# Kernel tuning notes

Measured on AMD Instinct MI355X. Metric: run time of the kernel, lower is better.

Reference implementation:

```python
import jax, jax.numpy as jnp
import numpy as np

D_MODEL = 768
N_HEADS = 12
D_K = D_MODEL // N_HEADS


def setup_inputs() -> dict:
    key = jax.random.key(0)
    ks = jax.random.split(key, 11)
    B, S, D = 8, 1024, D_MODEL
    std = 1.0 / np.sqrt(D)
    inp = {
        "key": jax.random.normal(ks[0], (B, S, D), jnp.float32),
        "query": jax.random.normal(ks[1], (B, S, D), jnp.float32),
        "value": jax.random.normal(ks[2], (B, S, D), jnp.float32),
        # torch.nn.Linear weights are [out, in]; y = x @ W.T + b
        "Wk": jax.random.uniform(ks[3], (D, D), jnp.float32, -std, std),
        "bk": jax.random.uniform(ks[4], (D,), jnp.float32, -std, std),
        "Wq": jax.random.uniform(ks[5], (D, D), jnp.float32, -std, std),
        "bq": jax.random.uniform(ks[6], (D,), jnp.float32, -std, std),
        "Wv": jax.random.uniform(ks[7], (D, D), jnp.float32, -std, std),
        "bv": jax.random.uniform(ks[8], (D,), jnp.float32, -std, std),
        "Wo": jax.random.uniform(ks[9], (D, D), jnp.float32, -std, std),
        "bo": jax.random.uniform(ks[10], (D,), jnp.float32, -std, std),
    }
    return inp


def _split_heads(x):
    B, S, D = x.shape
    return x.reshape(B, S, N_HEADS, D_K).transpose(0, 2, 1, 3)  # [B,H,S,d_k]


def reference(key, query, value, Wk, bk, Wq, bq, Wv, bv, Wo, bo):
    k = _split_heads(key @ Wk.T + bk)
    q = _split_heads(query @ Wq.T + bq)
    v = _split_heads(value @ Wv.T + bv)
    scores = jnp.einsum("bhqd,bhkd->bhqk", q, k) / jnp.sqrt(jnp.float32(D_K))
    attn = jax.nn.softmax(scores, axis=-1)
    out = jnp.einsum("bhqk,bhkd->bhqd", attn, v)  # [B,H,S,d_k]
    B, H, S, dk = out.shape
    concat = out.transpose(0, 2, 1, 3).reshape(B, S, H * dk)
    return concat @ Wo.T + bo
```

## Files before the change

kernel.cpp:

```cpp
#include <hip/hip_runtime.h>
#include <stdint.h>

#define DI __device__ __forceinline__

typedef __attribute__((ext_vector_type(8))) __bf16 bfrag;
typedef __attribute__((ext_vector_type(4))) __bf16 bf16x4;
typedef __attribute__((ext_vector_type(4))) float f32x4;

static constexpr int Bb = 8, Ss = 1024, Dd = 768, Hh = 12, DKk = 64;
static constexpr int Mm = Bb * Ss;

typedef __attribute__((address_space(3))) void lds_void_t;
typedef const __attribute__((address_space(1))) void gvoid_t;

DI void async_load16(const void* g, void* lds) {
    __builtin_amdgcn_global_load_lds((gvoid_t*)(uintptr_t)g,
                                     (lds_void_t*)(uint32_t)(uintptr_t)lds, 16, 0, 0);
}

#if __has_builtin(__builtin_amdgcn_exp2f)
#define EXP2(x) __builtin_amdgcn_exp2f(x)
#else
extern "C" __device__ float __ocml_exp2_f32(float);
#define EXP2(x) __ocml_exp2_f32(x)
#endif

__global__ __launch_bounds__(256) void cvt_k(const float* __restrict__ a0, const float* __restrict__ a1,
                                             const float* __restrict__ a2,
                                             const float* __restrict__ w0, const float* __restrict__ w1,
                                             const float* __restrict__ w2, const float* __restrict__ w3,
                                             __bf16* __restrict__ da0, __bf16* __restrict__ da1,
                                             __bf16* __restrict__ da2,
                                             __bf16* __restrict__ dw0, __bf16* __restrict__ dw1,
                                             __bf16* __restrict__ dw2, __bf16* __restrict__ dw3) {
    const int bid = (int)blockIdx.x;
    const float* s; __bf16* d; int off;
    if (bid < 9216) {
        const int ti = bid / 3072;
        off = (bid % 3072) * 2048;
        s = ti == 0 ? a0 : ti == 1 ? a1 : a2;
        d = ti == 0 ? da0 : ti == 1 ? da1 : da2;
    } else {
        const int b2 = bid - 9216;
        const int ti = b2 / 288;
        off = (b2 % 288) * 2048;
        s = ti == 0 ? w0 : ti == 1 ? w1 : ti == 2 ? w2 : w3;
        d = ti == 0 ? dw0 : ti == 1 ? dw1 : ti == 2 ? dw2 : dw3;
    }
    const int i = off + (int)threadIdx.x * 8;
    f32x4 a = *(const f32x4*)(s + i);
    f32x4 b = *(const f32x4*)(s + i + 4);
    bfrag o;
#pragma unroll
    for (int j = 0; j < 4; ++j) { o[j] = (__bf16)a[j]; o[j + 4] = (__bf16)b[j]; }
    *(bfrag*)(d + i) = o;
}

DI void gemm_core8(const __bf16* __restrict__ A, const __bf16* __restrict__ W,
                   __bf16* As, __bf16* Bs, int row0, int col0, int t, f32x4 acc[4][2]) {
    const int lane = t & 63, w = t >> 6;
    const int l15 = lane & 15, lg = lane >> 4;
    const int wr = (w >> 2) * 64, wc = (w & 3) * 32;
    const int rl = lane >> 3, clin = lane & 7;

    for (int k0 = 0; k0 < 768; k0 += 64) {
        __syncthreads();
#pragma unroll
        for (int o = 0; o < 2; ++o) {
            const int g = w * 2 + o;
            const int r = g * 8 + rl;
            const int cg = clin ^ (r & 7);
            async_load16(A + (size_t)(row0 + r) * Dd + k0 + cg * 8, As + g * 512);
            async_load16(W + (size_t)(col0 + r) * Dd + k0 + cg * 8, Bs + g * 512);
        }
        __syncthreads();

        bfrag af[4][2], bf[2][2];
#pragma unroll
        for (int mi = 0; mi < 4; ++mi) {
            const int ra = wr + mi * 16 + l15;
#pragma unroll
            for (int ks = 0; ks < 2; ++ks)
                af[mi][ks] = *(const bfrag*)(As + ra * 64 + (((ks * 4 + lg) ^ (ra & 7)) * 8));
        }
#pragma unroll
        for (int ni = 0; ni < 2; ++ni) {
            const int rb = wc + ni * 16 + l15;
#pragma unroll
            for (int ks = 0; ks < 2; ++ks)
                bf[ni][ks] = *(const bfrag*)(Bs + rb * 64 + (((ks * 4 + lg) ^ (rb & 7)) * 8));
        }
#pragma unroll
        for (int mi = 0; mi < 4; ++mi)
#pragma unroll
            for (int ni = 0; ni < 2; ++ni)
#pragma unroll
                for (int ks = 0; ks < 2; ++ks)
                    acc[mi][ni] = __builtin_amdgcn_mfma_f32_16x16x32_bf16(af[mi][ks], bf[ni][ks],
                                                                          acc[mi][ni], 0, 0, 0);
    }
}

__global__ __launch_bounds__(512) void qkv_gemm(const __bf16* __restrict__ qA, const __bf16* __restrict__ kA,
                                                const __bf16* __restrict__ vA,
                                                const __bf16* __restrict__ qW, const __bf16* __restrict__ kW,
                                                const __bf16* __restrict__ vW,
                                                const float* __restrict__ qb, const float* __restrict__ kb,
                                                const float* __restrict__ vb,
                                                __bf16* __restrict__ qO, __bf16* __restrict__ kO,
                                                __bf16* __restrict__ vO) {
    __shared__ __attribute__((aligned(16))) char smem[32768];
    __bf16* As = (__bf16*)smem;
    __bf16* Bs = (__bf16*)(smem + 16384);

    const int h = (int)blockIdx.x;
    const int l = (h & 7) * 144 + (h >> 3);
    const int z = l / 384, r2 = l % 384;
    const int row0 = (r2 / 6) * 128, col0 = (r2 % 6) * 128;

    const __bf16* A = z == 0 ? qA : z == 1 ? kA : vA;
    const __bf16* W = z == 0 ? qW : z == 1 ? kW : vW;
    const float* bias = z == 0 ? qb : z == 1 ? kb : vb;
    __bf16* O = z == 0 ? qO : z == 1 ? kO : vO;

    const int t = (int)threadIdx.x;
    const int lane = t & 63, w = t >> 6;
    const int l15 = lane & 15, lg = lane >> 4;
    const int wr = (w >> 2) * 64, wc = (w & 3) * 32;

    f32x4 acc[4][2] = {};
    gemm_core8(A, W, As, Bs, row0, col0, t, acc);

    if (z == 2) {
        auto T = reinterpret_cast<__bf16(*)[136]>(smem);
        const int bb2 = row0 >> 10, sb = row0 & 1023;
#pragma unroll
        for (int dh = 0; dh < 2; ++dh) {
            __syncthreads();
            if (((w >> 1) & 1) == dh) {
#pragma unroll
                for (int mi = 0; mi < 4; ++mi)
#pragma unroll
                    for (int ni = 0; ni < 2; ++ni) {
                        const int dcol = (w & 1) * 32 + ni * 16 + l15;
                        const float bv = bias[col0 + dh * 64 + dcol];
#pragma unroll
                        for (int j = 0; j < 4; ++j)
                            T[dcol][wr + mi * 16 + lg * 4 + j] = (__bf16)(acc[mi][ni][j] + bv);
                    }
            }
            __syncthreads();
#pragma unroll
            for (int it = 0; it < 2; ++it) {
                const int ld = it * 32 + (t >> 4);
                const int cs = (t & 15) * 8;
                const int col = col0 + dh * 64 + ld;
                const int head = col >> 6, dd = col & 63;
                __bf16* dst = O + ((size_t)(bb2 * Hh + head) * DKk + dd) * Ss + sb + cs;
                *reinterpret_cast<bfrag*>(dst) = *reinterpret_cast<const bfrag*>(&T[ld][cs]);
            }
        }
    } else {
        const float scl = (z == 0) ? 0.18033688f : 1.0f;
#pragma unroll
        for (int mi = 0; mi < 4; ++mi) {
#pragma unroll
            for (int ni = 0; ni < 2; ++ni) {
                const int cg = col0 + wc + ni * 16 + l15;
                const float bv = bias[cg];
#pragma unroll
                for (int j = 0; j < 4; ++j) {
                    const int rg = row0 + wr + mi * 16 + lg * 4 + j;
                    const float val = (acc[mi][ni][j] + bv) * scl;
                    const int bb = rg >> 10, ss = rg & 1023;
                    const int hh2 = cg >> 6, dd = cg & 63;
                    O[((size_t)(bb * Hh + hh2) * Ss + ss) * DKk + dd] = (__bf16)val;
                }
            }
        }
    }
}

__global__ __launch_bounds__(512) void o_gemm(const __bf16* __restrict__ A, const __bf16* __restrict__ W,
                                              const float* __restrict__ bias, float* __restrict__ Out) {
    __shared__ __attribute__((aligned(16))) char smem[24576];
    __bf16* As = (__bf16*)smem;
    __bf16* Bs = (__bf16*)(smem + 16384);

    const int h = (int)blockIdx.x;
    const int l = (h & 7) * 96 + (h >> 3);
    const int row0 = (l / 12) * 128, col0 = (l % 12) * 64;

    const int t = (int)threadIdx.x;
    const int lane = t & 63, w = t >> 6;
    const int l15 = lane & 15, lg = lane >> 4;
    const int wr = (w >> 1) * 32, wc = (w & 1) * 32;
    const int rl = lane >> 3, clin = lane & 7;

    f32x4 acc[2][2] = {};

    for (int k0 = 0; k0 < 768; k0 += 64) {
        __syncthreads();
#pragma unroll
        for (int o = 0; o < 2; ++o) {
            const int g = w * 2 + o;
            const int r = g * 8 + rl;
            const int cg = clin ^ (r & 7);
            async_load16(A + (size_t)(row0 + r) * Dd + k0 + cg * 8, As + g * 512);
        }
        {
            const int r = w * 8 + rl;
            const int cg = clin ^ (r & 7);
            async_load16(W + (size_t)(col0 + r) * Dd + k0 + cg * 8, Bs + w * 512);
        }
        __syncthreads();

        bfrag af[2][2], bf[2][2];
#pragma unroll
        for (int mi = 0; mi < 2; ++mi) {
            const int ra = wr + mi * 16 + l15;
#pragma unroll
            for (int ks = 0; ks < 2; ++ks)
                af[mi][ks] = *(const bfrag*)(As + ra * 64 + (((ks * 4 + lg) ^ (ra & 7)) * 8));
        }
#pragma unroll
        for (int ni = 0; ni < 2; ++ni) {
            const int rb = wc + ni * 16 + l15;
#pragma unroll
            for (int ks = 0; ks < 2; ++ks)
                bf[ni][ks] = *(const bfrag*)(Bs + rb * 64 + (((ks * 4 + lg) ^ (rb & 7)) * 8));
        }
#pragma unroll
        for (int mi = 0; mi < 2; ++mi)
#pragma unroll
            for (int ni = 0; ni < 2; ++ni)
#pragma unroll
                for (int ks = 0; ks < 2; ++ks)
                    acc[mi][ni] = __builtin_amdgcn_mfma_f32_16x16x32_bf16(af[mi][ks], bf[ni][ks],
                                                                          acc[mi][ni], 0, 0, 0);
    }

#pragma unroll
    for (int mi = 0; mi < 2; ++mi) {
#pragma unroll
        for (int ni = 0; ni < 2; ++ni) {
            const int cg = col0 + wc + ni * 16 + l15;
            const float bv = bias[cg];
#pragma unroll
            for (int j = 0; j < 4; ++j) {
                const int rg = row0 + wr + mi * 16 + lg * 4 + j;
                Out[(size_t)rg * Dd + cg] = acc[mi][ni][j] + bv;
            }
        }
    }
}

__global__ __launch_bounds__(512) void attn_k(const __bf16* __restrict__ q,
                                              const __bf16* __restrict__ k,
                                              const __bf16* __restrict__ vt,
                                              __bf16* __restrict__ o) {
    __shared__ __attribute__((aligned(16))) __bf16 Ks[64][72];
    __shared__ __attribute__((aligned(16))) __bf16 Vs[64][72];
    __shared__ __attribute__((aligned(16))) __bf16 plds[8][16][72];
    const int t = (int)threadIdx.x;
    const int lane = t & 63, w = t >> 6;
    const int l15 = lane & 15, lg = lane >> 4;
    const int blk = (int)blockIdx.x;
    const int bh = blk % 96, qt = blk / 96;
    const size_t bhb = (size_t)bh * Ss;
    const __bf16* qp = q + bhb * DKk;
    const __bf16* kp = k + bhb * DKk;
    const __bf16* vtp = vt + bhb * DKk;
    const int qbase = qt * 128 + w * 16;
    const int srow = t >> 3, sc = (t & 7) * 8;

    bfrag bq[2];
#pragma unroll
    for (int ks = 0; ks < 2; ++ks)
        bq[ks] = *reinterpret_cast<const bfrag*>(qp + (size_t)(qbase + l15) * DKk + ks * 32 + lg * 8);

    float lpart = 0.f;
    f32x4 oacc[4] = {};

    {
        bfrag k0 = *reinterpret_cast<const bfrag*>(kp + (size_t)srow * DKk + sc);
        bfrag v0 = *reinterpret_cast<const bfrag*>(vtp + (size_t)srow * Ss + sc);
        *reinterpret_cast<bfrag*>(&Ks[srow][sc]) = k0;
        *reinterpret_cast<bfrag*>(&Vs[srow][sc]) = v0;
    }
    __syncthreads();

    for (int kt = 0; kt < 16; ++kt) {
        bfrag kn, vn;
        if (kt < 15) {
            const int kb1 = (kt + 1) * 64;
            kn = *reinterpret_cast<const bfrag*>(kp + (size_t)(kb1 + srow) * DKk + sc);
            vn = *reinterpret_cast<const bfrag*>(vtp + (size_t)srow * Ss + kb1 + sc);
        }

        f32x4 sacc[4] = {};
        __builtin_amdgcn_s_setprio(1);
#pragma unroll
        for (int n = 0; n < 4; ++n) {
#pragma unroll
            for (int ks = 0; ks < 2; ++ks) {
                const bfrag ak = *reinterpret_cast<const bfrag*>(&Ks[n * 16 + l15][ks * 32 + lg * 8]);
                sacc[n] = __builtin_amdgcn_mfma_f32_16x16x32_bf16(ak, bq[ks], sacc[n], 0, 0, 0);
            }
        }
        __builtin_amdgcn_s_setprio(0);

        __syncthreads();
        if (kt < 15)
            *reinterpret_cast<bfrag*>(&Ks[srow][sc]) = kn;

        float p[4][4];
        float rs = 0.f;
#pragma unroll
        for (int n = 0; n < 4; ++n)
#pragma unroll
            for (int j = 0; j < 4; ++j) {
                const float pe = EXP2(sacc[n][j]);
                p[n][j] = pe;
                rs += pe;
            }
        lpart += rs;

#pragma unroll
        for (int n = 0; n < 4; ++n) {
            bf16x4 pk;
#pragma unroll
            for (int j = 0; j < 4; ++j) pk[j] = (__bf16)p[n][j];
            *reinterpret_cast<bf16x4*>(&plds[w][l15][n * 16 + lg * 4]) = pk;
        }

        __builtin_amdgcn_s_setprio(1);
#pragma unroll
        for (int ks = 0; ks < 2; ++ks) {
            const bfrag ap = *reinterpret_cast<const bfrag*>(&plds[w][l15][ks * 32 + lg * 8]);
#pragma unroll
            for (int dt = 0; dt < 4; ++dt) {
                const bfrag bv = *reinterpret_cast<const bfrag*>(&Vs[dt * 16 + l15][ks * 32 + lg * 8]);
                oacc[dt] = __builtin_amdgcn_mfma_f32_16x16x32_bf16(ap, bv, oacc[dt], 0, 0, 0);
            }
        }
        __builtin_amdgcn_s_setprio(0);

        __syncthreads();
        if (kt < 15)
            *reinterpret_cast<bfrag*>(&Vs[srow][sc]) = vn;
    }

    float lrow = lpart;
    lrow += __shfl_xor(lrow, 16);
    lrow += __shfl_xor(lrow, 32);
    float linv[4];
#pragma unroll
    for (int j = 0; j < 4; ++j) linv[j] = 1.0f / __shfl(lrow, lg * 4 + j);
    const int bb = bh / Hh, hh = bh % Hh;
#pragma unroll
    for (int dt = 0; dt < 4; ++dt)
#pragma unroll
        for (int j = 0; j < 4; ++j) {
            const int qrow = qbase + lg * 4 + j;
            o[((size_t)(bb * Ss + qrow)) * Dd + hh * DKk + dt * 16 + l15] =
                (__bf16)(oacc[dt][j] * linv[j]);
        }
}

extern "C" void kernel_launch(void* const* d_in, const int* in_sizes, int n_in,
                              void* d_out, int out_size, void* d_ws, size_t ws_size,
                              hipStream_t stream) {
    (void)in_sizes; (void)n_in; (void)out_size; (void)ws_size;
    const float* key   = (const float*)d_in[0];
    const float* query = (const float*)d_in[1];
    const float* value = (const float*)d_in[2];
    const float* Wk = (const float*)d_in[3];
    const float* bk = (const float*)d_in[4];
    const float* Wq = (const float*)d_in[5];
    const float* bq = (const float*)d_in[6];
    const float* Wv = (const float*)d_in[7];
    const float* bvp = (const float*)d_in[8];
    const float* Wo = (const float*)d_in[9];
    const float* bo = (const float*)d_in[10];

    const size_t NA = (size_t)Mm * Dd;
    const size_t NW = (size_t)Dd * Dd;
    __bf16* p = (__bf16*)d_ws;
    __bf16* qab = p;            p += NA;
    __bf16* kab = p;            p += NA;
    __bf16* vab = p;            p += NA;
    __bf16* wqb = p;            p += NW;
    __bf16* wkb = p;            p += NW;
    __bf16* wvb = p;            p += NW;
    __bf16* wob = p;            p += NW;
    __bf16* qws = p;            p += NA;
    __bf16* kws = p;            p += NA;
    __bf16* vtws = p;           p += NA;
    __bf16* aws = qab;

    dim3 b256(256), b512(512);
    cvt_k<<<dim3(10368), b256, 0, stream>>>(query, key, value, Wq, Wk, Wv, Wo,
                                            qab, kab, vab, wqb, wkb, wvb, wob);
    qkv_gemm<<<dim3(1152), b512, 0, stream>>>(qab, kab, vab,
                                              wqb, wkb, wvb,
                                              bq, bk, bvp,
                                              qws, kws, vtws);
    attn_k<<<dim3(Ss / 128 * Hh * Bb), b512, 0, stream>>>(qws, kws, vtws, aws);
    o_gemm<<<dim3(768), b512, 0, stream>>>(aws, wob, bo, (float*)d_out);
}
```

Baseline: 109.1 us.

## Fuse fp32-to-bf16 activation conversion into QKV GEMM A-tile loads

The separate conversion pass over the three fp32 activation tensors is removed. The QKV GEMM now reads fp32 activations directly, converts them to bf16 in registers and writes them swizzled into LDS, while weights are still pre-converted and loaded asynchronously. This saves a full write and re-read of three bf16 activation copies. The cost is that A-tile loads become synchronous register loads rather than async global-to-LDS copies, and each GEMM block re-reads and re-converts fp32 data across its six column tiles.

After: 110.2 us. No clear change (+1.0%).

```diff
diff --git a/kernel.cpp b/kernel.cpp
--- a/kernel.cpp
+++ b/kernel.cpp
@@ -25,29 +25,15 @@
 #define EXP2(x) __ocml_exp2_f32(x)
 #endif
 
-__global__ __launch_bounds__(256) void cvt_k(const float* __restrict__ a0, const float* __restrict__ a1,
-                                             const float* __restrict__ a2,
-                                             const float* __restrict__ w0, const float* __restrict__ w1,
-                                             const float* __restrict__ w2, const float* __restrict__ w3,
-                                             __bf16* __restrict__ da0, __bf16* __restrict__ da1,
-                                             __bf16* __restrict__ da2,
-                                             __bf16* __restrict__ dw0, __bf16* __restrict__ dw1,
-                                             __bf16* __restrict__ dw2, __bf16* __restrict__ dw3) {
+__global__ __launch_bounds__(256) void cvtw_k(const float* __restrict__ w0, const float* __restrict__ w1,
+                                              const float* __restrict__ w2, const float* __restrict__ w3,
+                                              __bf16* __restrict__ d0, __bf16* __restrict__ d1,
+                                              __bf16* __restrict__ d2, __bf16* __restrict__ d3) {
     const int bid = (int)blockIdx.x;
-    const float* s; __bf16* d; int off;
-    if (bid < 9216) {
-        const int ti = bid / 3072;
-        off = (bid % 3072) * 2048;
-        s = ti == 0 ? a0 : ti == 1 ? a1 : a2;
-        d = ti == 0 ? da0 : ti == 1 ? da1 : da2;
-    } else {
-        const int b2 = bid - 9216;
-        const int ti = b2 / 288;
-        off = (b2 % 288) * 2048;
-        s = ti == 0 ? w0 : ti == 1 ? w1 : ti == 2 ? w2 : w3;
-        d = ti == 0 ? dw0 : ti == 1 ? dw1 : ti == 2 ? dw2 : dw3;
-    }
-    const int i = off + (int)threadIdx.x * 8;
+    const int ti = bid / 288;
+    const int i = (bid % 288) * 2048 + (int)threadIdx.x * 8;
+    const float* s = ti == 0 ? w0 : ti == 1 ? w1 : ti == 2 ? w2 : w3;
+    __bf16* d = ti == 0 ? d0 : ti == 1 ? d1 : ti == 2 ? d2 : d3;
     f32x4 a = *(const f32x4*)(s + i);
     f32x4 b = *(const f32x4*)(s + i + 4);
     bfrag o;
@@ -101,8 +87,8 @@
     }
 }
 
-__global__ __launch_bounds__(512) void qkv_gemm(const __bf16* __restrict__ qA, const __bf16* __restrict__ kA,
-                                                const __bf16* __restrict__ vA,
+__global__ __launch_bounds__(512) void qkv_gemm(const float* __restrict__ qA, const float* __restrict__ kA,
+                                                const float* __restrict__ vA,
                                                 const __bf16* __restrict__ qW, const __bf16* __restrict__ kW,
                                                 const __bf16* __restrict__ vW,
                                                 const float* __restrict__ qb, const float* __restrict__ kb,
@@ -118,7 +104,7 @@
     const int z = l / 384, r2 = l % 384;
     const int row0 = (r2 / 6) * 128, col0 = (r2 % 6) * 128;
 
-    const __bf16* A = z == 0 ? qA : z == 1 ? kA : vA;
+    const float* A = z == 0 ? qA : z == 1 ? kA : vA;
     const __bf16* W = z == 0 ? qW : z == 1 ? kW : vW;
     const float* bias = z == 0 ? qb : z == 1 ? kb : vb;
     __bf16* O = z == 0 ? qO : z == 1 ? kO : vO;
@@ -127,9 +113,59 @@
     const int lane = t & 63, w = t >> 6;
     const int l15 = lane & 15, lg = lane >> 4;
     const int wr = (w >> 2) * 64, wc = (w & 3) * 32;
+    const int rl = lane >> 3, clin = lane & 7;
+    const int rw = t >> 2, c2 = (t & 3) * 2;
 
     f32x4 acc[4][2] = {};
-    gemm_core8(A, W, As, Bs, row0, col0, t, acc);
+
+    for (int k0 = 0; k0 < 768; k0 += 64) {
+        __syncthreads();
+        const float* srcA = A + (size_t)(row0 + rw) * Dd + k0 + c2 * 8;
+        f32x4 a0 = *(const f32x4*)(srcA);
+        f32x4 a1 = *(const f32x4*)(srcA + 4);
+        f32x4 a2 = *(const f32x4*)(srcA + 8);
+        f32x4 a3 = *(const f32x4*)(srcA + 12);
+#pragma unroll
+        for (int o = 0; o < 2; ++o) {
+            const int g = w * 2 + o;
+            const int r = g * 8 + rl;
+            const int cg = clin ^ (r & 7);
+            async_load16(W + (size_t)(col0 + r) * Dd + k0 + cg * 8, Bs + g * 512);
+        }
+        bfrag o0, o1;
+#pragma unroll
+        for (int j = 0; j < 4; ++j) {
+            o0[j] = (__bf16)a0[j]; o0[j + 4] = (__bf16)a1[j];
+            o1[j] = (__bf16)a2[j]; o1[j + 4] = (__bf16)a3[j];
+        }
+        *(bfrag*)(As + rw * 64 + ((c2 ^ (rw & 7)) * 8)) = o0;
+        *(bfrag*)(As + rw * 64 + (((c2 + 1) ^ (rw & 7)) * 8)) = o1;
+        __syncthreads();
+
+        bfrag af[4][2], bf[2][2];
+#pragma unroll
+        for (int mi = 0; mi < 4; ++mi) {
+            const int ra = wr + mi * 16 + l15;
+#pragma unroll
+            for (int ks = 0; ks < 2; ++ks)
+                af[mi][ks] = *(const bfrag*)(As + ra * 64 + (((ks * 4 + lg) ^ (ra & 7)) * 8));
+        }
+#pragma unroll
+        for (int ni = 0; ni < 2; ++ni) {
+            const int rb = wc + ni * 16 + l15;
+#pragma unroll
+            for (int ks = 0; ks < 2; ++ks)
+                bf[ni][ks] = *(const bfrag*)(Bs + rb * 64 + (((ks * 4 + lg) ^ (rb & 7)) * 8));
+        }
+#pragma unroll
+        for (int mi = 0; mi < 4; ++mi)
+#pragma unroll
+            for (int ni = 0; ni < 2; ++ni)
+#pragma unroll
+                for (int ks = 0; ks < 2; ++ks)
+                    acc[mi][ni] = __builtin_amdgcn_mfma_f32_16x16x32_bf16(af[mi][ks], bf[ni][ks],
+                                                                          acc[mi][ni], 0, 0, 0);
+    }
 
     if (z == 2) {
         auto T = reinterpret_cast<__bf16(*)[136]>(smem);
@@ -387,9 +423,6 @@
     const size_t NA = (size_t)Mm * Dd;
     const size_t NW = (size_t)Dd * Dd;
     __bf16* p = (__bf16*)d_ws;
-    __bf16* qab = p;            p += NA;
-    __bf16* kab = p;            p += NA;
-    __bf16* vab = p;            p += NA;
     __bf16* wqb = p;            p += NW;
     __bf16* wkb = p;            p += NW;
     __bf16* wvb = p;            p += NW;
@@ -397,12 +430,11 @@
     __bf16* qws = p;            p += NA;
     __bf16* kws = p;            p += NA;
     __bf16* vtws = p;           p += NA;
-    __bf16* aws = qab;
+    __bf16* aws = p;            p += NA;
 
     dim3 b256(256), b512(512);
-    cvt_k<<<dim3(10368), b256, 0, stream>>>(query, key, value, Wq, Wk, Wv, Wo,
-                                            qab, kab, vab, wqb, wkb, wvb, wob);
-    qkv_gemm<<<dim3(1152), b512, 0, stream>>>(qab, kab, vab,
+    cvtw_k<<<dim3(1152), b256, 0, stream>>>(Wq, Wk, Wv, Wo, wqb, wkb, wvb, wob);
+    qkv_gemm<<<dim3(1152), b512, 0, stream>>>(query, key, value,
                                               wqb, wkb, wvb,
                                               bq, bk, bvp,
                                               qws, kws, vtws);
```

## Fuse fp32-to-bf16 activation conversion into QKV GEMM loads

Applied to the files above, without the earlier changes.

The separate conversion pass over the three fp32 activation tensors is removed. The QKV GEMM now async-loads fp32 A tiles straight into LDS and converts them to bf16 while building MFMA fragments, which avoids writing and re-reading a bf16 copy of the activations. To fit fp32 A tiles in the same LDS budget, the row tile drops from 128 to 64, doubling the grid. This may cost some data reuse and adds conversion ALU work in the inner loop.

Result: slower. 113.2 us (+3.8%).

```diff
diff --git a/kernel.cpp b/kernel.cpp
--- a/kernel.cpp
+++ b/kernel.cpp
@@ -25,29 +25,15 @@
 #define EXP2(x) __ocml_exp2_f32(x)
 #endif
 
-__global__ __launch_bounds__(256) void cvt_k(const float* __restrict__ a0, const float* __restrict__ a1,
-                                             const float* __restrict__ a2,
-                                             const float* __restrict__ w0, const float* __restrict__ w1,
-                                             const float* __restrict__ w2, const float* __restrict__ w3,
-                                             __bf16* __restrict__ da0, __bf16* __restrict__ da1,
-                                             __bf16* __restrict__ da2,
-                                             __bf16* __restrict__ dw0, __bf16* __restrict__ dw1,
-                                             __bf16* __restrict__ dw2, __bf16* __restrict__ dw3) {
+__global__ __launch_bounds__(256) void cvtw_k(const float* __restrict__ w0, const float* __restrict__ w1,
+                                              const float* __restrict__ w2, const float* __restrict__ w3,
+                                              __bf16* __restrict__ d0, __bf16* __restrict__ d1,
+                                              __bf16* __restrict__ d2, __bf16* __restrict__ d3) {
     const int bid = (int)blockIdx.x;
-    const float* s; __bf16* d; int off;
-    if (bid < 9216) {
-        const int ti = bid / 3072;
-        off = (bid % 3072) * 2048;
-        s = ti == 0 ? a0 : ti == 1 ? a1 : a2;
-        d = ti == 0 ? da0 : ti == 1 ? da1 : da2;
-    } else {
-        const int b2 = bid - 9216;
-        const int ti = b2 / 288;
-        off = (b2 % 288) * 2048;
-        s = ti == 0 ? w0 : ti == 1 ? w1 : ti == 2 ? w2 : w3;
-        d = ti == 0 ? dw0 : ti == 1 ? dw1 : ti == 2 ? dw2 : dw3;
-    }
-    const int i = off + (int)threadIdx.x * 8;
+    const int ti = bid / 288;
+    const int i = (bid % 288) * 2048 + (int)threadIdx.x * 8;
+    const float* s = ti == 0 ? w0 : ti == 1 ? w1 : ti == 2 ? w2 : w3;
+    __bf16* d = ti == 0 ? d0 : ti == 1 ? d1 : ti == 2 ? d2 : d3;
     f32x4 a = *(const f32x4*)(s + i);
     f32x4 b = *(const f32x4*)(s + i + 4);
     bfrag o;
@@ -56,53 +42,8 @@
     *(bfrag*)(d + i) = o;
 }
 
-DI void gemm_core8(const __bf16* __restrict__ A, const __bf16* __restrict__ W,
-                   __bf16* As, __bf16* Bs, int row0, int col0, int t, f32x4 acc[4][2]) {
-    const int lane = t & 63, w = t >> 6;
-    const int l15 = lane & 15, lg = lane >> 4;
-    const int wr = (w >> 2) * 64, wc = (w & 3) * 32;
-    const int rl = lane >> 3, clin = lane & 7;
-
-    for (int k0 = 0; k0 < 768; k0 += 64) {
-        __syncthreads();
-#pragma unroll
-        for (int o = 0; o < 2; ++o) {
-            const int g = w * 2 + o;
-            const int r = g * 8 + rl;
-            const int cg = clin ^ (r & 7);
-            async_load16(A + (size_t)(row0 + r) * Dd + k0 + cg * 8, As + g * 512);
-            async_load16(W + (size_t)(col0 + r) * Dd + k0 + cg * 8, Bs + g * 512);
-        }
-        __syncthreads();
-
-        bfrag af[4][2], bf[2][2];
-#pragma unroll
-        for (int mi = 0; mi < 4; ++mi) {
-            const int ra = wr + mi * 16 + l15;
-#pragma unroll
-            for (int ks = 0; ks < 2; ++ks)
-                af[mi][ks] = *(const bfrag*)(As + ra * 64 + (((ks * 4 + lg) ^ (ra & 7)) * 8));
-        }
-#pragma unroll
-        for (int ni = 0; ni < 2; ++ni) {
-            const int rb = wc + ni * 16 + l15;
-#pragma unroll
-            for (int ks = 0; ks < 2; ++ks)
-                bf[ni][ks] = *(const bfrag*)(Bs + rb * 64 + (((ks * 4 + lg) ^ (rb & 7)) * 8));
-        }
-#pragma unroll
-        for (int mi = 0; mi < 4; ++mi)
-#pragma unroll
-            for (int ni = 0; ni < 2; ++ni)
-#pragma unroll
-                for (int ks = 0; ks < 2; ++ks)
-                    acc[mi][ni] = __builtin_amdgcn_mfma_f32_16x16x32_bf16(af[mi][ks], bf[ni][ks],
-                                                                          acc[mi][ni], 0, 0, 0);
-    }
-}
-
-__global__ __launch_bounds__(512) void qkv_gemm(const __bf16* __restrict__ qA, const __bf16* __restrict__ kA,
-                                                const __bf16* __restrict__ vA,
+__global__ __launch_bounds__(512) void qkv_gemm(const float* __restrict__ qA, const float* __restrict__ kA,
+                                                const float* __restrict__ vA,
                                                 const __bf16* __restrict__ qW, const __bf16* __restrict__ kW,
                                                 const __bf16* __restrict__ vW,
                                                 const float* __restrict__ qb, const float* __restrict__ kb,
@@ -110,15 +51,15 @@
                                                 __bf16* __restrict__ qO, __bf16* __restrict__ kO,
                                                 __bf16* __restrict__ vO) {
     __shared__ __attribute__((aligned(16))) char smem[32768];
-    __bf16* As = (__bf16*)smem;
+    float* Asf = (float*)smem;
     __bf16* Bs = (__bf16*)(smem + 16384);
 
     const int h = (int)blockIdx.x;
-    const int l = (h & 7) * 144 + (h >> 3);
-    const int z = l / 384, r2 = l % 384;
-    const int row0 = (r2 / 6) * 128, col0 = (r2 % 6) * 128;
-
-    const __bf16* A = z == 0 ? qA : z == 1 ? kA : vA;
+    const int l = (h & 7) * 288 + (h >> 3);
+    const int z = l / 768, r2 = l % 768;
+    const int row0 = (r2 / 6) * 64, col0 = (r2 % 6) * 128;
+
+    const float* A = z == 0 ? qA : z == 1 ? kA : vA;
     const __bf16* W = z == 0 ? qW : z == 1 ? kW : vW;
     const float* bias = z == 0 ? qb : z == 1 ? kb : vb;
     __bf16* O = z == 0 ? qO : z == 1 ? kO : vO;
@@ -126,55 +67,101 @@
     const int t = (int)threadIdx.x;
     const int lane = t & 63, w = t >> 6;
     const int l15 = lane & 15, lg = lane >> 4;
-    const int wr = (w >> 2) * 64, wc = (w & 3) * 32;
-
-    f32x4 acc[4][2] = {};
-    gemm_core8(A, W, As, Bs, row0, col0, t, acc);
+    const int wm = w >> 2, wn = w & 3;
+    const int rl = lane >> 3, clin = lane & 7;
+    const int ra4 = lane >> 4, ca = lane & 15;
+
+    f32x4 acc[2][2] = {};
+
+    for (int k0 = 0; k0 < 768; k0 += 64) {
+        __syncthreads();
+#pragma unroll
+        for (int o = 0; o < 2; ++o) {
+            const int g = w * 2 + o;
+            const int r = g * 4 + ra4;
+            const int cg = ca ^ (r & 7);
+            async_load16(A + (size_t)(row0 + r) * Dd + k0 + cg * 4, Asf + g * 256);
+        }
+#pragma unroll
+        for (int o = 0; o < 2; ++o) {
+            const int g = w * 2 + o;
+            const int r = g * 8 + rl;
+            const int cg = clin ^ (r & 7);
+            async_load16(W + (size_t)(col0 + r) * Dd + k0 + cg * 8, Bs + g * 512);
+        }
+        __syncthreads();
+
+        bfrag af[2][2], bf[2][2];
+#pragma unroll
+        for (int mi = 0; mi < 2; ++mi) {
+            const int ra = wm * 32 + mi * 16 + l15;
+#pragma unroll
+            for (int ks = 0; ks < 2; ++ks) {
+                const int c0 = ks * 8 + lg * 2;
+                const f32x4 v0 = *(const f32x4*)(Asf + ra * 64 + ((c0 ^ (ra & 7)) * 4));
+                const f32x4 v1 = *(const f32x4*)(Asf + ra * 64 + (((c0 + 1) ^ (ra & 7)) * 4));
+                bfrag f;
+#pragma unroll
+                for (int j = 0; j < 4; ++j) { f[j] = (__bf16)v0[j]; f[j + 4] = (__bf16)v1[j]; }
+                af[mi][ks] = f;
+            }
+        }
+#pragma unroll
+        for (int ni = 0; ni < 2; ++ni) {
+            const int rb = wn * 32 + ni * 16 + l15;
+#pragma unroll
+            for (int ks = 0; ks < 2; ++ks)
+                bf[ni][ks] = *(const bfrag*)(Bs + rb * 64 + (((ks * 4 + lg) ^ (rb & 7)) * 8));
+        }
+#pragma unroll
+        for (int mi = 0; mi < 2; ++mi)
+#pragma unroll
+            for (int ni = 0; ni < 2; ++ni)
+#pragma unroll
+                for (int ks = 0; ks < 2; ++ks)
+                    acc[mi][ni] = __builtin_amdgcn_mfma_f32_16x16x32_bf16(af[mi][ks], bf[ni][ks],
+                                                                          acc[mi][ni], 0, 0, 0);
+    }
 
     if (z == 2) {
-        auto T = reinterpret_cast<__bf16(*)[136]>(smem);
+        __syncthreads();
+        auto T = reinterpret_cast<__bf16(*)[72]>(smem);
         const int bb2 = row0 >> 10, sb = row0 & 1023;
 #pragma unroll
-        for (int dh = 0; dh < 2; ++dh) {
-            __syncthreads();
-            if (((w >> 1) & 1) == dh) {
-#pragma unroll
-                for (int mi = 0; mi < 4; ++mi)
-#pragma unroll
-                    for (int ni = 0; ni < 2; ++ni) {
-                        const int dcol = (w & 1) * 32 + ni * 16 + l15;
-                        const float bv = bias[col0 + dh * 64 + dcol];
-#pragma unroll
-                        for (int j = 0; j < 4; ++j)
-                            T[dcol][wr + mi * 16 + lg * 4 + j] = (__bf16)(acc[mi][ni][j] + bv);
-                    }
-            }
-            __syncthreads();
-#pragma unroll
-            for (int it = 0; it < 2; ++it) {
-                const int ld = it * 32 + (t >> 4);
-                const int cs = (t & 15) * 8;
-                const int col = col0 + dh * 64 + ld;
-                const int head = col >> 6, dd = col & 63;
-                __bf16* dst = O + ((size_t)(bb2 * Hh + head) * DKk + dd) * Ss + sb + cs;
-                *reinterpret_cast<bfrag*>(dst) = *reinterpret_cast<const bfrag*>(&T[ld][cs]);
-            }
+        for (int mi = 0; mi < 2; ++mi)
+#pragma unroll
+            for (int ni = 0; ni < 2; ++ni) {
+                const int dcol = wn * 32 + ni * 16 + l15;
+                const float bv = bias[col0 + dcol];
+#pragma unroll
+                for (int j = 0; j < 4; ++j)
+                    T[dcol][wm * 32 + mi * 16 + lg * 4 + j] = (__bf16)(acc[mi][ni][j] + bv);
+            }
+        __syncthreads();
+        {
+            const int d = t >> 2;
+            const int sch = (t & 3) * 16;
+            const int col = col0 + d;
+            const int head = col >> 6, dd = col & 63;
+            __bf16* dst = O + ((size_t)(bb2 * Hh + head) * DKk + dd) * Ss + sb + sch;
+            *reinterpret_cast<bfrag*>(dst) = *reinterpret_cast<const bfrag*>(&T[d][sch]);
+            *reinterpret_cast<bfrag*>(dst + 8) = *reinterpret_cast<const bfrag*>(&T[d][sch + 8]);
         }
     } else {
         const float scl = (z == 0) ? 0.18033688f : 1.0f;
 #pragma unroll
-        for (int mi = 0; mi < 4; ++mi) {
+        for (int mi = 0; mi < 2; ++mi) {
 #pragma unroll
             for (int ni = 0; ni < 2; ++ni) {
-                const int cg = col0 + wc + ni * 16 + l15;
+                const int cg = col0 + wn * 32 + ni * 16 + l15;
                 const float bv = bias[cg];
+                const int head = cg >> 6, dd = cg & 63;
 #pragma unroll
                 for (int j = 0; j < 4; ++j) {
-                    const int rg = row0 + wr + mi * 16 + lg * 4 + j;
-                    const float val = (acc[mi][ni][j] + bv) * scl;
+                    const int rg = row0 + wm * 32 + mi * 16 + lg * 4 + j;
                     const int bb = rg >> 10, ss = rg & 1023;
-                    const int hh2 = cg >> 6, dd = cg & 63;
-                    O[((size_t)(bb * Hh + hh2) * Ss + ss) * DKk + dd] = (__bf16)val;
+                    O[((size_t)(bb * Hh + head) * Ss + ss) * DKk + dd] =
+                        (__bf16)((acc[mi][ni][j] + bv) * scl);
                 }
             }
         }
@@ -387,9 +374,6 @@
     const size_t NA = (size_t)Mm * Dd;
     const size_t NW = (size_t)Dd * Dd;
     __bf16* p = (__bf16*)d_ws;
-    __bf16* qab = p;            p += NA;
-    __bf16* kab = p;            p += NA;
-    __bf16* vab = p;            p += NA;
     __bf16* wqb = p;            p += NW;
     __bf16* wkb = p;            p += NW;
     __bf16* wvb = p;            p += NW;
@@ -397,12 +381,11 @@
     __bf16* qws = p;            p += NA;
     __bf16* kws = p;            p += NA;
     __bf16* vtws = p;           p += NA;
-    __bf16* aws = qab;
+    __bf16* aws = p;            p += NA;
 
     dim3 b256(256), b512(512);
-    cvt_k<<<dim3(10368), b256, 0, stream>>>(query, key, value, Wq, Wk, Wv, Wo,
-                                            qab, kab, vab, wqb, wkb, wvb, wob);
-    qkv_gemm<<<dim3(1152), b512, 0, stream>>>(qab, kab, vab,
+    cvtw_k<<<dim3(1152), b256, 0, stream>>>(Wq, Wk, Wv, Wo, wqb, wkb, wvb, wob);
+    qkv_gemm<<<dim3(2304), b512, 0, stream>>>(query, key, value,
                                               wqb, wkb, wvb,
                                               bq, bk, bvp,
                                               qws, kws, vtws);
```
